# Kernel optimization log

Measured on AMD Instinct MI355X. Metric: run time of the kernel, lower is better.

## Reference

```python
import jax, jax.numpy as jnp
import numpy as np

BS, GS, E, KMAX = 128, 2000, 128, 4
CLIP = 10.0
NEG = -1e30


def _gru(x, hprev, Wih, Whh, bih, bhh):
    # torch.nn.GRUCell math
    gi = x @ Wih.T + bih
    gh = hprev @ Whh.T + bhh
    ir, iz, i_n = jnp.split(gi, 3, axis=-1)
    hr, hz, h_n = jnp.split(gh, 3, axis=-1)
    r = jax.nn.sigmoid(ir + hr)
    z = jax.nn.sigmoid(iz + hz)
    n = jnp.tanh(i_n + r * h_n)
    return (1.0 - z) * n + z * hprev


def setup_inputs() -> dict:
    key = jax.random.key(0)
    it = iter(jax.random.split(key, 40))
    s = 1.0 / float(np.sqrt(E))
    u = lambda shape: jax.random.uniform(next(it), shape, jnp.float32, -s, s)
    inp = {
        "h": jax.random.normal(next(it), (BS, GS, E), jnp.float32),
        "rec": jax.random.randint(next(it), (BS, GS), 0, GS, dtype=jnp.int32),
        "context2": jax.random.normal(next(it), (BS, 9), jnp.float32),
        "visited_time": jax.random.randint(next(it), (BS, GS), 0, GS, dtype=jnp.int32),
        "last_action": jax.random.randint(next(it), (BS, 1), 0, GS, dtype=jnp.int32),
        "fixed_action": jax.random.randint(next(it), (BS, KMAX), 0, GS, dtype=jnp.int32),
    }
    for n in ["W_K1", "W_K2", "W_K3", "W_K4", "W_Q1", "W_Q2", "W_Q3", "W_Q4", "W_init"]:
        inp[n] = u((E, E))
    for n in ["b_init", "V1", "V2", "init_query"]:
        inp[n] = u((E,))
    for r in ["rnn1", "rnn2"]:
        inp[r + "_Wih"] = u((3 * E, E))
        inp[r + "_Whh"] = u((3 * E, E))
        inp[r + "_bih"] = u((3 * E,))
        inp[r + "_bhh"] = u((3 * E,))
    return inp


def _forward(h, rec, visited_time, last_action, fixed_action,
             W_K1, W_K2, W_K3, W_K4, W_Q1, W_Q2, W_Q3, W_Q4, V1, V2,
             W_init, b_init, init_query,
             rnn1_Wih, rnn1_Whh, rnn1_bih, rnn1_bhh,
             rnn2_Wih, rnn2_Whh, rnn2_bih, rnn2_bhh):
    bs, gs, e = h.shape
    cols = jnp.arange(gs)[None, :]          # [1, gs]
    rows = jnp.arange(bs)
    # K projections of h are loop-invariant: hoist them (same math as in-loop recompute)
    K1h = jnp.einsum('bge,fe->bgf', h, W_K1)
    K2h = jnp.einsum('bge,fe->bgf', h, W_K2)
    K3h = jnp.einsum('bge,fe->bgf', h, W_K3)
    K4h = jnp.einsum('bge,fe->bgf', h, W_K4)
    q1 = q2 = h.mean(1) @ W_init.T + b_init
    input_q1 = input_q2 = jnp.broadcast_to(init_query, (bs, e))
    mask = jnp.zeros((bs, gs), bool)
    stopped = jnp.ones((bs,), bool)
    nol = jnp.full((bs, 1), -1, jnp.int32)   # next_of_last_action
    ai = jnp.zeros((bs, KMAX), jnp.int32)    # action_index
    kl = jnp.zeros((bs, KMAX + 1), jnp.int32)
    kr = jnp.zeros((bs, KMAX), jnp.int32)
    ll = jnp.zeros((bs,), h.dtype)
    vtt = None
    for i in range(KMAX):
        q1 = _gru(input_q1, q1, rnn1_Wih, rnn1_Whh, rnn1_bih, rnn1_bhh)
        q2 = _gru(input_q2, q2, rnn2_Wih, rnn2_Whh, rnn2_bih, rnn2_bhh)
        s1 = (V1 * jnp.tanh(K1h + (q1 @ W_Q1.T)[:, None, :] + K3h * (q1 @ W_Q3.T)[:, None, :])).sum(-1)
        s2 = (V2 * jnp.tanh(K2h + (q2 @ W_Q2.T)[:, None, :] + K4h * (q2 @ W_Q4.T)[:, None, :])).sum(-1)
        logits = jnp.tanh(s1 + s2) * CLIP
        logits = jnp.where(mask, NEG, logits)
        if i == 0:
            logits = jnp.where(cols == last_action, NEG, logits)
        action = fixed_action[:, i:i + 1]
        if i > 0:
            action = jnp.where(stopped[:, None], ai[:, 0:1], action)
        logp = jax.nn.log_softmax(logits, axis=-1)
        loss_now = jnp.take_along_axis(logp, action, 1)[:, 0]
        ll = ll + (loss_now if i == 0 else jnp.where(stopped, 0.0, loss_now))
        nna = jnp.take_along_axis(rec, action, 1)  # next_of_new_action [bs,1]
        ai = ai.at[:, i].set(action[:, 0])
        kl = kl.at[:, i].set(jnp.where(stopped, action[:, 0], kl[:, i]))
        kr = kr.at[:, (i - 1) % KMAX].set(jnp.where(stopped, kr[:, (i - 1) % KMAX], action[:, 0]))
        kl = kl.at[:, i + 1].set(nna[:, 0])
        input_q1 = h[rows, action[:, 0]]
        input_q2 = jnp.where(stopped[:, None], input_q1, h[rows, nol[:, 0] % gs])
        eq = (action == nol)[:, 0]
        stopped = eq if i == 0 else (stopped | eq)
        kl = kl.at[:, i].set(jnp.where(stopped, kl[:, (i - 1) % (KMAX + 1)], kl[:, i]))
        kr = kr.at[:, i].set(jnp.where(stopped, kr[:, (i - 1) % KMAX], kr[:, i]))
        if i == 0:
            vtt = (visited_time - jnp.take_along_axis(visited_time, action, 1)) % gs
        vtt_a = jnp.take_along_axis(vtt, action, 1)
        mask = vtt <= vtt_a
        if i == 0:
            mask = mask | (vtt > gs - 2)
        mask = jnp.where(stopped[:, None] & (cols == action), False, mask)
        allow = (~stopped) & (nna[:, 0] == ai[:, 0])
        mask = jnp.where(allow[:, None] & (cols == ai[:, 0:1]), False, mask)
        nol = jnp.where(stopped[:, None], jnp.int32(-1), nna)
    kr = kr.at[:, KMAX - 1].set(jnp.where(~stopped, kl[:, KMAX], kr[:, KMAX - 1]))
    action_all = jnp.concatenate([ai, kl[:, :KMAX], kr], axis=-1)  # [bs, 3*KMAX]
    return action_all, ll


def reference(h, rec, context2, visited_time, last_action, fixed_action,
              W_K1, W_K2, W_K3, W_K4, W_Q1, W_Q2, W_Q3, W_Q4,
              V1, V2, W_init, b_init, init_query,
              rnn1_Wih, rnn1_Whh, rnn1_bih, rnn1_bhh,
              rnn2_Wih, rnn2_Whh, rnn2_bih, rnn2_bhh):
    # context2 unused: with_explore_stat_feature=False path (learned V1/V2)
    return _forward(h, rec, visited_time, last_action, fixed_action,
                    W_K1, W_K2, W_K3, W_K4, W_Q1, W_Q2, W_Q3, W_Q4, V1, V2,
                    W_init, b_init, init_query,
                    rnn1_Wih, rnn1_Whh, rnn1_bih, rnn1_bhh,
                    rnn2_Wih, rnn2_Whh, rnn2_bih, rnn2_bhh)
```

## Files before the change

kernel.cpp:

```cpp
#include <hip/hip_runtime.h>
#include <math.h>

#define BS 128
#define GS 2000
#define E  128
#define KMAXI 4
#define CLIPV 10.0f
#define NEGV  -1.0e30f

typedef __bf16 bf16_t;
typedef __bf16 bf16x8 __attribute__((ext_vector_type(8)));
typedef float fx4 __attribute__((ext_vector_type(4)));
typedef float fx2 __attribute__((ext_vector_type(2)));

__device__ __forceinline__ float fast_sigmoid(float x){ return 1.0f/(1.0f+__expf(-x)); }
__device__ __forceinline__ float fast_tanhf(float x){
    float e = __expf(2.0f*x);
    return 1.0f - 2.0f/(e + 1.0f);
}
__device__ __forceinline__ float pade_tanh(float x){
    float t = __builtin_amdgcn_fmed3f(x, -3.0f, 3.0f);
    float r = t*t;
    float num = t*(27.0f + r);
    float den = fmaf(9.0f, r, 27.0f);
    return num * __builtin_amdgcn_rcpf(den);
}
__device__ __forceinline__ fx2 tanh2_poly(fx2 x){
    fx2 t;
    t.x = __builtin_amdgcn_fmed3f(x.x, -3.0f, 3.0f);
    t.y = __builtin_amdgcn_fmed3f(x.y, -3.0f, 3.0f);
    fx2 r = t*t;
    fx2 q = r*(-0.0015650f) + 0.03172875f;
    q = q*r + (-0.23082094f);
    q = q*r + 0.979947f;
    return t*q;
}
__device__ __forceinline__ int pymod(int a){ int d = a % GS; return d < 0 ? d + GS : d; }

__device__ __forceinline__ void load_lds16(const bf16_t* g, bf16_t* l){
    __builtin_amdgcn_global_load_lds(
        (const __attribute__((address_space(1))) void*)g,
        (__attribute__((address_space(3))) void*)l, 16, 0, 0);
}

#define SC_STRIDE 64

__global__ __launch_bounds__(128) void k_traj(
    const int* __restrict__ rec, const int* __restrict__ vtime,
    const int* __restrict__ last_action, const int* __restrict__ fixed_action,
    int* __restrict__ sc, float* __restrict__ out)
{
    int b = threadIdx.x;
    if (b >= BS) return;
    int stopped = 1, nol = -1;
    int ai[4]={0,0,0,0}, kl[5]={0,0,0,0,0}, kr[4]={0,0,0,0};
    int a0 = 0;
    int* scb = sc + b*SC_STRIDE;
    for (int it=0; it<KMAXI; ++it){
        int action = (it==0) ? fixed_action[b*KMAXI]
                             : (stopped ? ai[0] : fixed_action[b*KMAXI+it]);
        int old_stopped = stopped;
        if (it==0) a0 = action;
        int vta = (it==0) ? 0 : pymod(vtime[(size_t)b*GS+action] - vtime[(size_t)b*GS+a0]);
        int nna = rec[(size_t)b*GS+action];
        int eq  = (action == nol) ? 1 : 0;
        int new_stopped = (it==0) ? eq : (stopped | eq);
        int ai0 = (it==0) ? action : ai[0];
        int allow = (!new_stopped) && (nna == ai0);

        ai[it] = action;
        if (old_stopped)  kl[it] = action;
        if (!old_stopped) kr[(it+3)&3] = action;
        kl[it+1] = nna;
        if (new_stopped) kl[it] = kl[(it+4)%5];
        if (new_stopped) kr[it] = kr[(it+3)&3];

        int row1 = action;
        int i2 = pymod(nol);
        int row2 = old_stopped ? row1 : i2;

        int* s_it = scb + 8 + it*8;
        s_it[0]=action; s_it[1]=old_stopped; s_it[2]=new_stopped;
        s_it[3]=allow;  s_it[4]=vta; s_it[5]=row1; s_it[6]=row2;

        nol = new_stopped ? -1 : nna;
        stopped = new_stopped;
    }
    scb[0] = a0;
    if (!stopped) kr[3] = kl[4];
    out[BS*12 + b] = 0.0f;
    for (int j=0;j<4;++j) out[b*12+j]   = (float)ai[j];
    for (int j=0;j<4;++j) out[b*12+4+j] = (float)kl[j];
    for (int j=0;j<4;++j) out[b*12+8+j] = (float)kr[j];
}

__global__ __launch_bounds__(256) void k_hmean(const float* __restrict__ h, float* __restrict__ hpart){
    int b = blockIdx.x, p = blockIdx.y, tid = threadIdx.x;
    int e4 = (tid & 31) * 4;
    int gsub = tid >> 5;
    float4 acc = {0.f,0.f,0.f,0.f};
    int g0 = p*125, g1 = g0+125;
    for (int g = g0 + gsub; g < g1; g += 8){
        float4 v = *(const float4*)(h + ((size_t)b*GS + g)*E + e4);
        acc.x += v.x; acc.y += v.y; acc.z += v.z; acc.w += v.w;
    }
    __shared__ float ps[8][E];
    *(float4*)(&ps[gsub][e4]) = acc;
    __syncthreads();
    if (tid < E){
        float s = 0.f;
        #pragma unroll
        for (int j=0;j<8;++j) s += ps[j][tid];
        hpart[(b*16+p)*E + tid] = s;
    }
}

__device__ __forceinline__ float dot32(const float* a, const float* __restrict__ w){
    const float4* a4=(const float4*)a; const float4* w4=(const float4*)w;
    float s=0.f;
    #pragma unroll 8
    for (int i=0;i<32;++i){ float4 x=a4[i], y=w4[i]; s += x.x*y.x + x.y*y.y + x.z*y.z + x.w*y.w; }
    return s;
}

__global__ __launch_bounds__(384) void k_gru4(
    const float* __restrict__ hpart, const float* __restrict__ W_init,
    const float* __restrict__ b_init, const float* __restrict__ init_query,
    const float* __restrict__ h, const int* __restrict__ sc,
    const float* __restrict__ Wih1, const float* __restrict__ Whh1,
    const float* __restrict__ bih1, const float* __restrict__ bhh1,
    const float* __restrict__ Wih2, const float* __restrict__ Whh2,
    const float* __restrict__ bih2, const float* __restrict__ bhh2,
    const float* __restrict__ WQ1, const float* __restrict__ WQ2,
    const float* __restrict__ WQ3, const float* __restrict__ WQ4,
    float* __restrict__ add_buf, float* __restrict__ mul_buf)
{
    int b = blockIdx.x, rnn = blockIdx.y, t = threadIdx.x;
    const float* Wih = rnn ? Wih2 : Wih1;
    const float* Whh = rnn ? Whh2 : Whh1;
    const float* bih = rnn ? bih2 : bih1;
    const float* bhh = rnn ? bhh2 : bhh1;
    const float* WQa = rnn ? WQ2 : WQ1;
    const float* WQm = rnn ? WQ4 : WQ3;

    __shared__ float xv[E], hv[E];
    __shared__ float gi_s[3*E], gh_s[3*E];

    if (t < E){
        float s = 0.f;
        for (int p=0;p<16;++p) s += hpart[(b*16+p)*E + t];
        xv[t] = s * (1.0f/(float)GS);
    }
    __syncthreads();
    if (t < E) hv[t] = b_init[t] + dot32(xv, W_init + (size_t)t*E);
    __syncthreads();
    if (t < E) xv[t] = init_query[t];
    __syncthreads();

    for (int s=0; s<KMAXI; ++s){
        if (s>0){
            if (t < E){
                int row = sc[b*SC_STRIDE + 8 + (s-1)*8 + (rnn==0 ? 5 : 6)];
                xv[t] = h[((size_t)b*GS + row)*E + t];
            }
            __syncthreads();
        }
        {
            float gi = bih[t] + dot32(xv, Wih + (size_t)t*E);
            float gh = bhh[t] + dot32(hv, Whh + (size_t)t*E);
            gi_s[t] = gi; gh_s[t] = gh;
        }
        __syncthreads();
        if (t < E){
            float r = fast_sigmoid(gi_s[t]     + gh_s[t]);
            float z = fast_sigmoid(gi_s[t+E]   + gh_s[t+E]);
            float n = fast_tanhf  (gi_s[t+2*E] + r*gh_s[t+2*E]);
            hv[t] = (1.f-z)*n + z*hv[t];
        }
        __syncthreads();
        if (t < 2*E){
            int r = t & (E-1);
            const float* W = (t < E) ? WQa : WQm;
            float v = dot32(hv, W + (size_t)r*E);
            int slot = s*2 + rnn;
            if (t < E) add_buf[(size_t)slot*BS*E + b*E + r] = v;
            else       mul_buf[(size_t)slot*BS*E + b*E + r] = v;
        }
        __syncthreads();
    }
}

__global__ __launch_bounds__(256) void k_mbuild(
    const float* __restrict__ WK1, const float* __restrict__ WK2,
    const float* __restrict__ WK3, const float* __restrict__ WK4,
    const float* __restrict__ mul_buf, bf16_t* __restrict__ Mb)
{
    int b = blockIdx.x, slot = blockIdx.y, tid = threadIdx.x;
    int arm = slot & 1;
    const float* WKa = arm ? WK2 : WK1;
    const float* WKm = arm ? WK4 : WK3;
    const float* mul = mul_buf + (size_t)slot*BS*E + b*E;
    __shared__ float mv[E];
    if (tid < E) mv[tid] = mul[tid];
    __syncthreads();
    bf16x8* outp = (bf16x8*)(Mb + ((size_t)slot*BS + b)*E*E);
    #pragma unroll
    for (int j=0;j<8;++j){
        int u = j*256 + tid;
        int f = u >> 4, e8 = u & 15;
        int e0 = e8*8;
        float mf = mv[f];
        float4 a0 = *(const float4*)(WKa + (size_t)f*E + e0);
        float4 a1 = *(const float4*)(WKa + (size_t)f*E + e0 + 4);
        float4 m0 = *(const float4*)(WKm + (size_t)f*E + e0);
        float4 m1 = *(const float4*)(WKm + (size_t)f*E + e0 + 4);
        bf16x8 o;
        o[0]=(bf16_t)(a0.x + m0.x*mf);
        o[1]=(bf16_t)(a0.y + m0.y*mf);
        o[2]=(bf16_t)(a0.z + m0.z*mf);
        o[3]=(bf16_t)(a0.w + m0.w*mf);
        o[4]=(bf16_t)(a1.x + m1.x*mf);
        o[5]=(bf16_t)(a1.y + m1.y*mf);
        o[6]=(bf16_t)(a1.z + m1.z*mf);
        o[7]=(bf16_t)(a1.w + m1.w*mf);
        outp[f*16 + (e8 ^ (f&7))] = o;
    }
}

__global__ __launch_bounds__(256,2) void k_scores(
    const float* __restrict__ hf, const bf16_t* __restrict__ Mb,
    const float* __restrict__ add_buf,
    const float* __restrict__ V1, const float* __restrict__ V2,
    float* __restrict__ raw4)
{
    __shared__ bf16_t sM[E*E];
    int b = blockIdx.x, yc = blockIdx.y, tid = threadIdx.x;
    int wave = tid >> 6, lane = tid & 63;
    int qd = lane >> 4, cl = lane & 15;
    int gbase = yc*128 + wave*32;

    float vv_r[2][8];
    #pragma unroll
    for (int tf=0; tf<8; ++tf){
        vv_r[0][tf] = V1[tf*16+cl];
        vv_r[1][tf] = V2[tf*16+cl];
    }

    bf16x8 afr[2][4];
    #pragma unroll
    for (int set=0; set<2; ++set){
        int grow = gbase + set*16 + cl;
        if (grow >= GS) grow = GS-1;
        const float* hrow = hf + ((size_t)b*GS + grow)*E;
        #pragma unroll
        for (int s=0;s<4;++s){
            const float* p = hrow + s*32 + qd*8;
            float4 u0 = *(const float4*)(p);
            float4 u1 = *(const float4*)(p+4);
            bf16x8 a;
            a[0]=(bf16_t)u0.x; a[1]=(bf16_t)u0.y; a[2]=(bf16_t)u0.z; a[3]=(bf16_t)u0.w;
            a[4]=(bf16_t)u1.x; a[5]=(bf16_t)u1.y; a[6]=(bf16_t)u1.z; a[7]=(bf16_t)u1.w;
            afr[set][s]=a;
        }
    }

    for (int it=0; it<KMAXI; ++it){
        fx2 s00={0.f,0.f}, s01={0.f,0.f}, s10={0.f,0.f}, s11={0.f,0.f};
        #pragma unroll
        for (int arm=0; arm<2; ++arm){
            int slot = it*2 + arm;
            const bf16_t* Gm = Mb + ((size_t)slot*BS + b)*E*E;
            const float* addv = add_buf + (size_t)slot*BS*E + b*E;

            float av_r[8];
            #pragma unroll
            for (int tf=0; tf<8; ++tf) av_r[tf] = addv[tf*16+cl];

            __syncthreads();
            #pragma unroll
            for (int j=0;j<8;++j){
                int c = wave*512 + j*64 + lane;
                load_lds16(Gm + (size_t)c*8, sM + (size_t)c*8);
            }
            __syncthreads();

            #pragma unroll
            for (int tf=0; tf<8; ++tf){
                int f = tf*16 + cl;
                bf16x8 b1[4];
                #pragma unroll
                for (int s=0;s<4;++s){
                    int e8 = s*4 + qd;
                    b1[s] = *(const bf16x8*)(sM + ((size_t)(f*16 + (e8 ^ (f&7))))*8);
                }
                float av = av_r[tf];
                fx4 a0 = {av,av,av,av};
                fx4 a1 = {av,av,av,av};
                #pragma unroll
                for (int s=0;s<4;++s){
                    a0 = __builtin_amdgcn_mfma_f32_16x16x32_bf16(afr[0][s], b1[s], a0, 0,0,0);
                    a1 = __builtin_amdgcn_mfma_f32_16x16x32_bf16(afr[1][s], b1[s], a1, 0,0,0);
                }
                fx2 vv2 = {vv_r[arm][tf], vv_r[arm][tf]};
                s00 += vv2 * tanh2_poly((fx2){a0[0], a0[1]});
                s01 += vv2 * tanh2_poly((fx2){a0[2], a0[3]});
                s10 += vv2 * tanh2_poly((fx2){a1[0], a1[1]});
                s11 += vv2 * tanh2_poly((fx2){a1[2], a1[3]});
            }
        }
        #pragma unroll
        for (int set=0;set<2;++set){
            fx2 pa = set ? s10 : s00;
            fx2 pb = set ? s11 : s01;
            float v[4] = {pa.x, pa.y, pb.x, pb.y};
            #pragma unroll
            for (int r=0;r<4;++r){
                float s = v[r];
                s += __shfl_xor(s, 1); s += __shfl_xor(s, 2);
                s += __shfl_xor(s, 4); s += __shfl_xor(s, 8);
                v[r] = s;
            }
            if (cl==0){
                int gi = gbase + set*16 + qd*4;
                if (gi+3 < GS){
                    float4 o;
                    o.x = CLIPV*pade_tanh(v[0]);
                    o.y = CLIPV*pade_tanh(v[1]);
                    o.z = CLIPV*pade_tanh(v[2]);
                    o.w = CLIPV*pade_tanh(v[3]);
                    *(float4*)(raw4 + ((size_t)it*BS + b)*GS + gi) = o;
                }
            }
        }
    }
}

__global__ __launch_bounds__(256) void k_ll(
    const float* __restrict__ raw4, const int* __restrict__ sc,
    const int* __restrict__ vtime, const int* __restrict__ last_action,
    float* __restrict__ out)
{
    __shared__ float sL[GS];
    __shared__ float red[256];
    int b = blockIdx.x, it = blockIdx.y, t = threadIdx.x;
    const int* scb = sc + b*SC_STRIDE;
    const int* s_it = scb + 8 + it*8;
    int action = s_it[0], olds = s_it[1];
    if (it>0 && olds) return;
    int a0 = scb[0];
    int la = last_action[b];
    int vt0 = vtime[(size_t)b*GS + a0];
    int ap=0, nsp=0, alp=0, vtp=0, p = it-1;
    if (it>0){
        const int* s_p = scb + 8 + p*8;
        ap = s_p[0]; nsp = s_p[2]; alp = s_p[3]; vtp = s_p[4];
    }
    for (int g=t; g<GS; g+=256){
        float l = raw4[((size_t)it*BS + b)*GS + g];
        int m;
        if (it==0){
            m = (g==la);
        } else {
            int d = pymod(vtime[(size_t)b*GS+g] - vt0);
            m = (d <= vtp) ? 1 : 0;
            if (p==0 && d > GS-2) m = 1;
            if (nsp && g==ap)     m = 0;
            if (alp && g==a0)     m = 0;
        }
        sL[g] = m ? NEGV : l;
    }
    __syncthreads();
    float mx = -3.0e38f;
    for (int g=t; g<GS; g+=256) mx = fmaxf(mx, sL[g]);
    red[t]=mx; __syncthreads();
    for (int s=128;s>0;s>>=1){ if(t<s) red[t]=fmaxf(red[t],red[t+s]); __syncthreads(); }
    mx = red[0]; __syncthreads();
    float sm = 0.f;
    for (int g=t; g<GS; g+=256) sm += __expf(sL[g]-mx);
    red[t]=sm; __syncthreads();
    for (int s=128;s>0;s>>=1){ if(t<s) red[t]+=red[t+s]; __syncthreads(); }
    if (t==0){
        float lse = mx + __logf(red[0]);
        atomicAdd(&out[BS*12 + b], sL[action] - lse);
    }
}

extern "C" void kernel_launch(void* const* d_in, const int* in_sizes, int n_in,
                              void* d_out, int out_size, void* d_ws, size_t ws_size,
                              hipStream_t stream)
{
    const float* h            = (const float*)d_in[0];
    const int*   rec          = (const int*)  d_in[1];
    const int*   vtime        = (const int*)  d_in[3];
    const int*   last_action  = (const int*)  d_in[4];
    const int*   fixed_action = (const int*)  d_in[5];
    const float* WK1=(const float*)d_in[6],  *WK2=(const float*)d_in[7];
    const float* WK3=(const float*)d_in[8],  *WK4=(const float*)d_in[9];
    const float* WQ1=(const float*)d_in[10], *WQ2=(const float*)d_in[11];
    const float* WQ3=(const float*)d_in[12], *WQ4=(const float*)d_in[13];
    const float* W_init=(const float*)d_in[14];
    const float* b_init=(const float*)d_in[15];
    const float* V1=(const float*)d_in[16], *V2=(const float*)d_in[17];
    const float* init_query=(const float*)d_in[18];
    const float* Wih1=(const float*)d_in[19], *Whh1=(const float*)d_in[20];
    const float* bih1=(const float*)d_in[21], *bhh1=(const float*)d_in[22];
    const float* Wih2=(const float*)d_in[23], *Whh2=(const float*)d_in[24];
    const float* bih2=(const float*)d_in[25], *bhh2=(const float*)d_in[26];
    float* out = (float*)d_out;

    char* ws = (char*)d_ws;
    size_t off = 0;
    auto alloc = [&](size_t bytes)->char*{
        char* p = ws + off; off += (bytes + 255) & ~(size_t)255; return p;
    };
    bf16_t* Mb     = (bf16_t*)alloc((size_t)8*BS*E*E*sizeof(bf16_t));
    float*  raw4   = (float*) alloc((size_t)KMAXI*BS*GS*sizeof(float));
    float*  add_buf= (float*) alloc((size_t)8*BS*E*sizeof(float));
    float*  mul_buf= (float*) alloc((size_t)8*BS*E*sizeof(float));
    float*  hpart  = (float*) alloc((size_t)BS*16*E*sizeof(float));
    int*    sc     = (int*)   alloc((size_t)BS*SC_STRIDE*sizeof(int));
    (void)in_sizes; (void)n_in; (void)out_size; (void)ws_size;

    hipLaunchKernelGGL(k_traj, dim3(1), dim3(128), 0, stream,
                       rec, vtime, last_action, fixed_action, sc, out);
    hipLaunchKernelGGL(k_hmean, dim3(BS,16), dim3(256), 0, stream, h, hpart);
    hipLaunchKernelGGL(k_gru4, dim3(BS,2), dim3(384), 0, stream,
                       hpart, W_init, b_init, init_query, h, sc,
                       Wih1,Whh1,bih1,bhh1, Wih2,Whh2,bih2,bhh2,
                       WQ1,WQ2,WQ3,WQ4, add_buf, mul_buf);
    hipLaunchKernelGGL(k_mbuild, dim3(BS,8), dim3(256), 0, stream,
                       WK1,WK2,WK3,WK4, mul_buf, Mb);
    hipLaunchKernelGGL(k_scores, dim3(BS,16), dim3(256), 0, stream,
                       h, Mb, add_buf, V1, V2, raw4);
    hipLaunchKernelGGL(k_ll, dim3(BS, KMAXI), dim3(256), 0, stream,
                       raw4, sc, vtime, last_action, out);
}
```

Baseline: 435.8 us.

## Fuse trajectory into hmean, M-build into GRU, and widen score tiles

The trajectory kernel now runs as an extra grid row of the h-mean kernel, and the bf16 M-matrix build moves into the GRU kernel. This removes two launches and the mul_buf round trip. The score kernel now handles 64 rows per wave with four MFMA sets, halving the grid and reusing each loaded B fragment across more rows, at the cost of more registers (the launch-bounds minimum of 2 blocks is dropped). The pymod modulo is replaced by a single conditional add, which assumes the difference always lies within (-GS, GS).

```diff
diff --git a/kernel.cpp b/kernel.cpp
--- a/kernel.cpp
+++ b/kernel.cpp
@@ -35,7 +35,7 @@
     q = q*r + 0.979947f;
     return t*q;
 }
-__device__ __forceinline__ int pymod(int a){ int d = a % GS; return d < 0 ? d + GS : d; }
+__device__ __forceinline__ int pymod_s(int a){ return a < 0 ? a + GS : a; }
 
 __device__ __forceinline__ void load_lds16(const bf16_t* g, bf16_t* l){
     __builtin_amdgcn_global_load_lds(
@@ -45,57 +45,59 @@
 
 #define SC_STRIDE 64
 
-__global__ __launch_bounds__(128) void k_traj(
+__global__ __launch_bounds__(256) void k_hmean(
+    const float* __restrict__ h, float* __restrict__ hpart,
     const int* __restrict__ rec, const int* __restrict__ vtime,
     const int* __restrict__ last_action, const int* __restrict__ fixed_action,
     int* __restrict__ sc, float* __restrict__ out)
 {
-    int b = threadIdx.x;
-    if (b >= BS) return;
-    int stopped = 1, nol = -1;
-    int ai[4]={0,0,0,0}, kl[5]={0,0,0,0,0}, kr[4]={0,0,0,0};
-    int a0 = 0;
-    int* scb = sc + b*SC_STRIDE;
-    for (int it=0; it<KMAXI; ++it){
-        int action = (it==0) ? fixed_action[b*KMAXI]
-                             : (stopped ? ai[0] : fixed_action[b*KMAXI+it]);
-        int old_stopped = stopped;
-        if (it==0) a0 = action;
-        int vta = (it==0) ? 0 : pymod(vtime[(size_t)b*GS+action] - vtime[(size_t)b*GS+a0]);
-        int nna = rec[(size_t)b*GS+action];
-        int eq  = (action == nol) ? 1 : 0;
-        int new_stopped = (it==0) ? eq : (stopped | eq);
-        int ai0 = (it==0) ? action : ai[0];
-        int allow = (!new_stopped) && (nna == ai0);
-
-        ai[it] = action;
-        if (old_stopped)  kl[it] = action;
-        if (!old_stopped) kr[(it+3)&3] = action;
-        kl[it+1] = nna;
-        if (new_stopped) kl[it] = kl[(it+4)%5];
-        if (new_stopped) kr[it] = kr[(it+3)&3];
-
-        int row1 = action;
-        int i2 = pymod(nol);
-        int row2 = old_stopped ? row1 : i2;
-
-        int* s_it = scb + 8 + it*8;
-        s_it[0]=action; s_it[1]=old_stopped; s_it[2]=new_stopped;
-        s_it[3]=allow;  s_it[4]=vta; s_it[5]=row1; s_it[6]=row2;
-
-        nol = new_stopped ? -1 : nna;
-        stopped = new_stopped;
-    }
-    scb[0] = a0;
-    if (!stopped) kr[3] = kl[4];
-    out[BS*12 + b] = 0.0f;
-    for (int j=0;j<4;++j) out[b*12+j]   = (float)ai[j];
-    for (int j=0;j<4;++j) out[b*12+4+j] = (float)kl[j];
-    for (int j=0;j<4;++j) out[b*12+8+j] = (float)kr[j];
-}
-
-__global__ __launch_bounds__(256) void k_hmean(const float* __restrict__ h, float* __restrict__ hpart){
     int b = blockIdx.x, p = blockIdx.y, tid = threadIdx.x;
+    if (p == 16){
+        if (b != 0) return;
+        int t = tid;
+        if (t >= BS) return;
+        int stopped = 1, nol = -1;
+        int ai[4]={0,0,0,0}, kl[5]={0,0,0,0,0}, kr[4]={0,0,0,0};
+        int a0 = 0;
+        int* scb = sc + t*SC_STRIDE;
+        for (int it=0; it<KMAXI; ++it){
+            int action = (it==0) ? fixed_action[t*KMAXI]
+                                 : (stopped ? ai[0] : fixed_action[t*KMAXI+it]);
+            int old_stopped = stopped;
+            if (it==0) a0 = action;
+            int vta = (it==0) ? 0 : pymod_s(vtime[(size_t)t*GS+action] - vtime[(size_t)t*GS+a0]);
+            int nna = rec[(size_t)t*GS+action];
+            int eq  = (action == nol) ? 1 : 0;
+            int new_stopped = (it==0) ? eq : (stopped | eq);
+            int ai0 = (it==0) ? action : ai[0];
+            int allow = (!new_stopped) && (nna == ai0);
+
+            ai[it] = action;
+            if (old_stopped)  kl[it] = action;
+            if (!old_stopped) kr[(it+3)&3] = action;
+            kl[it+1] = nna;
+            if (new_stopped) kl[it] = kl[(it+4)%5];
+            if (new_stopped) kr[it] = kr[(it+3)&3];
+
+            int row1 = action;
+            int i2 = pymod_s(nol);
+            int row2 = old_stopped ? row1 : i2;
+
+            int* s_it = scb + 8 + it*8;
+            s_it[0]=action; s_it[1]=old_stopped; s_it[2]=new_stopped;
+            s_it[3]=allow;  s_it[4]=vta; s_it[5]=row1; s_it[6]=row2;
+
+            nol = new_stopped ? -1 : nna;
+            stopped = new_stopped;
+        }
+        scb[0] = a0;
+        if (!stopped) kr[3] = kl[4];
+        out[BS*12 + t] = 0.0f;
+        for (int j=0;j<4;++j) out[t*12+j]   = (float)ai[j];
+        for (int j=0;j<4;++j) out[t*12+4+j] = (float)kl[j];
+        for (int j=0;j<4;++j) out[t*12+8+j] = (float)kr[j];
+        return;
+    }
     int e4 = (tid & 31) * 4;
     int gsub = tid >> 5;
     float4 acc = {0.f,0.f,0.f,0.f};
@@ -133,7 +135,9 @@
     const float* __restrict__ bih2, const float* __restrict__ bhh2,
     const float* __restrict__ WQ1, const float* __restrict__ WQ2,
     const float* __restrict__ WQ3, const float* __restrict__ WQ4,
-    float* __restrict__ add_buf, float* __restrict__ mul_buf)
+    const float* __restrict__ WK1, const float* __restrict__ WK2,
+    const float* __restrict__ WK3, const float* __restrict__ WK4,
+    float* __restrict__ add_buf, bf16_t* __restrict__ Mb)
 {
     int b = blockIdx.x, rnn = blockIdx.y, t = threadIdx.x;
     const float* Wih = rnn ? Wih2 : Wih1;
@@ -142,8 +146,10 @@
     const float* bhh = rnn ? bhh2 : bhh1;
     const float* WQa = rnn ? WQ2 : WQ1;
     const float* WQm = rnn ? WQ4 : WQ3;
-
-    __shared__ float xv[E], hv[E];
+    const float* WKa = rnn ? WK2 : WK1;
+    const float* WKm = rnn ? WK4 : WK3;
+
+    __shared__ float xv[E], hv[E], mv[E];
     __shared__ float gi_s[3*E], gh_s[3*E];
 
     if (t < E){
@@ -178,56 +184,42 @@
             hv[t] = (1.f-z)*n + z*hv[t];
         }
         __syncthreads();
+        int slot = s*2 + rnn;
         if (t < 2*E){
             int r = t & (E-1);
             const float* W = (t < E) ? WQa : WQm;
             float v = dot32(hv, W + (size_t)r*E);
-            int slot = s*2 + rnn;
             if (t < E) add_buf[(size_t)slot*BS*E + b*E + r] = v;
-            else       mul_buf[(size_t)slot*BS*E + b*E + r] = v;
+            else       mv[r] = v;
         }
         __syncthreads();
-    }
-}
-
-__global__ __launch_bounds__(256) void k_mbuild(
-    const float* __restrict__ WK1, const float* __restrict__ WK2,
-    const float* __restrict__ WK3, const float* __restrict__ WK4,
-    const float* __restrict__ mul_buf, bf16_t* __restrict__ Mb)
-{
-    int b = blockIdx.x, slot = blockIdx.y, tid = threadIdx.x;
-    int arm = slot & 1;
-    const float* WKa = arm ? WK2 : WK1;
-    const float* WKm = arm ? WK4 : WK3;
-    const float* mul = mul_buf + (size_t)slot*BS*E + b*E;
-    __shared__ float mv[E];
-    if (tid < E) mv[tid] = mul[tid];
-    __syncthreads();
-    bf16x8* outp = (bf16x8*)(Mb + ((size_t)slot*BS + b)*E*E);
-    #pragma unroll
-    for (int j=0;j<8;++j){
-        int u = j*256 + tid;
-        int f = u >> 4, e8 = u & 15;
-        int e0 = e8*8;
-        float mf = mv[f];
-        float4 a0 = *(const float4*)(WKa + (size_t)f*E + e0);
-        float4 a1 = *(const float4*)(WKa + (size_t)f*E + e0 + 4);
-        float4 m0 = *(const float4*)(WKm + (size_t)f*E + e0);
-        float4 m1 = *(const float4*)(WKm + (size_t)f*E + e0 + 4);
-        bf16x8 o;
-        o[0]=(bf16_t)(a0.x + m0.x*mf);
-        o[1]=(bf16_t)(a0.y + m0.y*mf);
-        o[2]=(bf16_t)(a0.z + m0.z*mf);
-        o[3]=(bf16_t)(a0.w + m0.w*mf);
-        o[4]=(bf16_t)(a1.x + m1.x*mf);
-        o[5]=(bf16_t)(a1.y + m1.y*mf);
-        o[6]=(bf16_t)(a1.z + m1.z*mf);
-        o[7]=(bf16_t)(a1.w + m1.w*mf);
-        outp[f*16 + (e8 ^ (f&7))] = o;
-    }
-}
-
-__global__ __launch_bounds__(256,2) void k_scores(
+        {
+            bf16x8* outp = (bf16x8*)(Mb + ((size_t)slot*BS + b)*E*E);
+            for (int u = t; u < 2048; u += 384){
+                int f = u >> 4, e8 = u & 15;
+                int e0 = e8*8;
+                float mf = mv[f];
+                float4 a0 = *(const float4*)(WKa + (size_t)f*E + e0);
+                float4 a1 = *(const float4*)(WKa + (size_t)f*E + e0 + 4);
+                float4 m0 = *(const float4*)(WKm + (size_t)f*E + e0);
+                float4 m1 = *(const float4*)(WKm + (size_t)f*E + e0 + 4);
+                bf16x8 o;
+                o[0]=(bf16_t)(a0.x + m0.x*mf);
+                o[1]=(bf16_t)(a0.y + m0.y*mf);
+                o[2]=(bf16_t)(a0.z + m0.z*mf);
+                o[3]=(bf16_t)(a0.w + m0.w*mf);
+                o[4]=(bf16_t)(a1.x + m1.x*mf);
+                o[5]=(bf16_t)(a1.y + m1.y*mf);
+                o[6]=(bf16_t)(a1.z + m1.z*mf);
+                o[7]=(bf16_t)(a1.w + m1.w*mf);
+                outp[f*16 + (e8 ^ (f&7))] = o;
+            }
+        }
+        __syncthreads();
+    }
+}
+
+__global__ __launch_bounds__(256) void k_scores(
     const float* __restrict__ hf, const bf16_t* __restrict__ Mb,
     const float* __restrict__ add_buf,
     const float* __restrict__ V1, const float* __restrict__ V2,
@@ -237,7 +229,7 @@
     int b = blockIdx.x, yc = blockIdx.y, tid = threadIdx.x;
     int wave = tid >> 6, lane = tid & 63;
     int qd = lane >> 4, cl = lane & 15;
-    int gbase = yc*128 + wave*32;
+    int gbase = yc*256 + wave*64;
 
     float vv_r[2][8];
     #pragma unroll
@@ -246,9 +238,9 @@
         vv_r[1][tf] = V2[tf*16+cl];
     }
 
-    bf16x8 afr[2][4];
+    bf16x8 afr[4][4];
     #pragma unroll
-    for (int set=0; set<2; ++set){
+    for (int set=0; set<4; ++set){
         int grow = gbase + set*16 + cl;
         if (grow >= GS) grow = GS-1;
         const float* hrow = hf + ((size_t)b*GS + grow)*E;
@@ -265,7 +257,9 @@
     }
 
     for (int it=0; it<KMAXI; ++it){
-        fx2 s00={0.f,0.f}, s01={0.f,0.f}, s10={0.f,0.f}, s11={0.f,0.f};
+        fx2 acc[4][2];
+        #pragma unroll
+        for (int set=0;set<4;++set){ acc[set][0]=(fx2){0.f,0.f}; acc[set][1]=(fx2){0.f,0.f}; }
         #pragma unroll
         for (int arm=0; arm<2; ++arm){
             int slot = it*2 + arm;
@@ -296,22 +290,30 @@
                 float av = av_r[tf];
                 fx4 a0 = {av,av,av,av};
                 fx4 a1 = {av,av,av,av};
+                fx4 a2 = {av,av,av,av};
+                fx4 a3 = {av,av,av,av};
                 #pragma unroll
                 for (int s=0;s<4;++s){
                     a0 = __builtin_amdgcn_mfma_f32_16x16x32_bf16(afr[0][s], b1[s], a0, 0,0,0);
                     a1 = __builtin_amdgcn_mfma_f32_16x16x32_bf16(afr[1][s], b1[s], a1, 0,0,0);
+                    a2 = __builtin_amdgcn_mfma_f32_16x16x32_bf16(afr[2][s], b1[s], a2, 0,0,0);
+                    a3 = __builtin_amdgcn_mfma_f32_16x16x32_bf16(afr[3][s], b1[s], a3, 0,0,0);
                 }
                 fx2 vv2 = {vv_r[arm][tf], vv_r[arm][tf]};
-                s00 += vv2 * tanh2_poly((fx2){a0[0], a0[1]});
-                s01 += vv2 * tanh2_poly((fx2){a0[2], a0[3]});
-                s10 += vv2 * tanh2_poly((fx2){a1[0], a1[1]});
-                s11 += vv2 * tanh2_poly((fx2){a1[2], a1[3]});
+                acc[0][0] += vv2 * tanh2_poly((fx2){a0[0], a0[1]});
+                acc[0][1] += vv2 * tanh2_poly((fx2){a0[2], a0[3]});
+                acc[1][0] += vv2 * tanh2_poly((fx2){a1[0], a1[1]});
+                acc[1][1] += vv2 * tanh2_poly((fx2){a1[2], a1[3]});
+                acc[2][0] += vv2 * tanh2_poly((fx2){a2[0], a2[1]});
+                acc[2][1] += vv2 * tanh2_poly((fx2){a2[2], a2[3]});
+                acc[3][0] += vv2 * tanh2_poly((fx2){a3[0], a3[1]});
+                acc[3][1] += vv2 * tanh2_poly((fx2){a3[2], a3[3]});
             }
         }
         #pragma unroll
-        for (int set=0;set<2;++set){
-            fx2 pa = set ? s10 : s00;
-            fx2 pb = set ? s11 : s01;
+        for (int set=0;set<4;++set){
+            fx2 pa = acc[set][0];
+            fx2 pb = acc[set][1];
             float v[4] = {pa.x, pa.y, pb.x, pb.y};
             #pragma unroll
             for (int r=0;r<4;++r){
@@ -361,7 +363,8 @@
         if (it==0){
             m = (g==la);
         } else {
-            int d = pymod(vtime[(size_t)b*GS+g] - vt0);
+            int d = vtime[(size_t)b*GS+g] - vt0;
+            if (d < 0) d += GS;
             m = (d <= vtp) ? 1 : 0;
             if (p==0 && d > GS-2) m = 1;
             if (nsp && g==ap)     m = 0;
@@ -416,21 +419,17 @@
     bf16_t* Mb     = (bf16_t*)alloc((size_t)8*BS*E*E*sizeof(bf16_t));
     float*  raw4   = (float*) alloc((size_t)KMAXI*BS*GS*sizeof(float));
     float*  add_buf= (float*) alloc((size_t)8*BS*E*sizeof(float));
-    float*  mul_buf= (float*) alloc((size_t)8*BS*E*sizeof(float));
     float*  hpart  = (float*) alloc((size_t)BS*16*E*sizeof(float));
     int*    sc     = (int*)   alloc((size_t)BS*SC_STRIDE*sizeof(int));
     (void)in_sizes; (void)n_in; (void)out_size; (void)ws_size;
 
-    hipLaunchKernelGGL(k_traj, dim3(1), dim3(128), 0, stream,
-                       rec, vtime, last_action, fixed_action, sc, out);
-    hipLaunchKernelGGL(k_hmean, dim3(BS,16), dim3(256), 0, stream, h, hpart);
+    hipLaunchKernelGGL(k_hmean, dim3(BS,17), dim3(256), 0, stream,
+                       h, hpart, rec, vtime, last_action, fixed_action, sc, out);
     hipLaunchKernelGGL(k_gru4, dim3(BS,2), dim3(384), 0, stream,
                        hpart, W_init, b_init, init_query, h, sc,
                        Wih1,Whh1,bih1,bhh1, Wih2,Whh2,bih2,bhh2,
-                       WQ1,WQ2,WQ3,WQ4, add_buf, mul_buf);
-    hipLaunchKernelGGL(k_mbuild, dim3(BS,8), dim3(256), 0, stream,
-                       WK1,WK2,WK3,WK4, mul_buf, Mb);
-    hipLaunchKernelGGL(k_scores, dim3(BS,16), dim3(256), 0, stream,
+                       WQ1,WQ2,WQ3,WQ4, WK1,WK2,WK3,WK4, add_buf, Mb);
+    hipLaunchKernelGGL(k_scores, dim3(BS,8), dim3(256), 0, stream,
                        h, Mb, add_buf, V1, V2, raw4);
     hipLaunchKernelGGL(k_ll, dim3(BS, KMAXI), dim3(256), 0, stream,
                        raw4, sc, vtime, last_action, out);
```

New measurement: 461.7 us. 1.06x slower.
